# Performance work log

Measured on AMD Instinct MI355X. Metric: run time of the kernel, lower is better.

Reference implementation:

```python
import jax, jax.numpy as jnp
import numpy as np

NOTES = 8192
NPB = 8          # notes per beat (max buffer size for beat attention)
BPM = 4          # beats per measure
BEATS = NOTES // NPB
MEAS = BEATS // BPM
NOTE_D = 512     # note.size*2 (bidirectional encoder output)
BEAT_D = 512     # beat.size*2
MEAS_D = 256     # measure.size*2
ENC = 128        # encoder.size
TEMPO_H = 256    # beat.size
FINAL_H = 256    # final.size
OUT = 11         # output_size
RES_D = 8        # 5 + 3
NEG = -1e30


def lstm_cell(x, h, c, Wih, Whh, b):
    z = x @ Wih.T + h @ Whh.T + b
    i, f, g, o = jnp.split(z, 4)
    c = jax.nn.sigmoid(f) * c + jax.nn.sigmoid(i) * jnp.tanh(g)
    h = jax.nn.sigmoid(o) * jnp.tanh(c)
    return h, c


def setup_inputs():
    key = jax.random.key(0)
    ks = iter(jax.random.split(key, 40))
    def rn(shape, s=1.0):
        return jax.random.normal(next(ks), shape, jnp.float32) * s
    TEMPO_IN = BEAT_D + MEAS_D + 1 + RES_D + (OUT - 1) + ENC  # 915
    FINAL_IN = NOTE_D + BEAT_D + MEAS_D + OUT + ENC           # 1419
    return {
        'note_emb': rn((1, NOTES, NOTE_D)),
        'beat_emb': rn((1, BEATS, BEAT_D)),
        'measure_emb': rn((1, MEAS, MEAS_D)),
        'perf_embedding': rn((1, 64)),
        'res_info': rn((1, BEATS, RES_D)),
        'sve_W': rn((ENC, 64), 0.05), 'sve_b': rn((ENC,), 0.05),
        'psm_Wih': rn((4 * ENC, MEAS_D + ENC), 0.05),
        'psm_Whh': rn((4 * ENC, ENC), 0.05),
        'psm_b': rn((4 * ENC,), 0.05),
        'mpf_W': rn((ENC, ENC), 0.05), 'mpf_b': rn((ENC,), 0.05),
        'att_W': rn((OUT - 1, OUT - 1), 0.05), 'att_b': rn((OUT - 1,), 0.05),
        'att_c': rn((OUT - 1,), 0.5),
        'tempo_Wih': rn((4 * TEMPO_H, TEMPO_IN), 0.05),
        'tempo_Whh': rn((4 * TEMPO_H, TEMPO_H), 0.05),
        'tempo_b': rn((4 * TEMPO_H,), 0.05),
        'tempo_fc_W': rn((1, TEMPO_H), 0.05), 'tempo_fc_b': rn((1,), 0.05),
        'out_Wih': rn((4 * FINAL_H, FINAL_IN), 0.05),
        'out_Whh': rn((4 * FINAL_H, FINAL_H), 0.05),
        'out_b': rn((4 * FINAL_H,), 0.05),
        'fc_W': rn((OUT - 1, FINAL_H), 0.05), 'fc_b': rn((OUT - 1,), 0.05),
        'beat_numbers': jnp.arange(NOTES, dtype=jnp.int32) // NPB,
        'measure_numbers': jnp.arange(NOTES, dtype=jnp.int32) // (NPB * BPM),
        'edges': jnp.zeros((1,), jnp.int32),
    }


def _forward(note_emb, beat_emb, measure_emb, perf_embedding, res_info,
             sve_W, sve_b, psm_Wih, psm_Whh, psm_b, mpf_W, mpf_b,
             att_W, att_b, att_c, tempo_Wih, tempo_Whh, tempo_b,
             tempo_fc_W, tempo_fc_b, out_Wih, out_Whh, out_b, fc_W, fc_b,
             beat_numbers, measure_numbers):
    dt = note_emb.dtype
    b_idx = beat_numbers - beat_numbers[0]
    m_idx = measure_numbers - measure_numbers[0]
    nbuf = att_W.shape[0]  # output_size - 1

    # style_vector_expandor (Dropout is identity at inference)
    z = jax.nn.relu(perf_embedding.reshape(-1) @ sve_W.T + sve_b)  # [ENC]

    # perform_style_to_measure LSTM over measures, then measure_perf_fc
    meas = measure_emb[0]  # [M, MEAS_D]
    pzm = jnp.concatenate([jnp.broadcast_to(z, (meas.shape[0], z.shape[0])), meas], axis=1)
    h0 = jnp.zeros(psm_Whh.shape[1], dt)
    def mstep(carry, x):
        h, c = carry
        h, c = lstm_cell(x, h, c, psm_Wih, psm_Whh, psm_b)
        return (h, c), h
    _, mps = jax.lax.scan(mstep, (h0, h0), pzm)
    mps = mps @ mpf_W.T + mpf_b  # [M, ENC] measure_perform_style

    # gather per-note context (pure memory traffic)
    beat_pn = beat_emb[0][b_idx]
    meas_pn = meas[m_idx]
    mps_pn = mps[m_idx]
    res_pn = res_info[0][b_idx]
    notes = note_emb[0]
    is_start = jnp.concatenate([jnp.ones((1,), bool), b_idx[1:] > b_idx[:-1]])

    th0 = jnp.zeros(tempo_Whh.shape[1], dt)
    fh0 = jnp.zeros(out_Whh.shape[1], dt)
    carry0 = (th0, th0, fh0, fh0, jnp.zeros((1,), dt), jnp.zeros((OUT,), dt),
              jnp.zeros((NPB, nbuf), dt), jnp.zeros((), jnp.int32))

    def step(carry, xs):
        th, tc, fh, fcc, prev_tempo, prev_out, buf, cnt = carry
        n_e, b_e, m_e, mp, r_e, start = xs
        # --- beat boundary: ContextAttention (1 head) over previous beat's fc outputs
        mask = jnp.arange(NPB) < cnt
        scores = jnp.tanh(buf @ att_W.T + att_b) @ att_c  # [NPB]
        w = jax.nn.softmax(jnp.where(mask, scores, NEG))
        result = jnp.where(cnt > 0, w @ buf, jnp.zeros((nbuf,), dt))
        cat_t = jnp.concatenate([b_e, m_e, prev_tempo, r_e, result, mp])
        nth, ntc = lstm_cell(cat_t, th, tc, tempo_Wih, tempo_Whh, tempo_b)
        new_tempo = nth @ tempo_fc_W.T + tempo_fc_b  # [1]
        th = jnp.where(start, nth, th)
        tc = jnp.where(start, ntc, tc)
        prev_tempo = jnp.where(start, new_tempo, prev_tempo)
        buf = jnp.where(start, jnp.zeros_like(buf), buf)
        cnt = jnp.where(start, 0, cnt)
        # --- per-note output LSTM step
        cat_o = jnp.concatenate([n_e, b_e, m_e, prev_out, mp])
        fh, fcc = lstm_cell(cat_o, fh, fcc, out_Wih, out_Whh, out_b)
        o = fh @ fc_W.T + fc_b  # [OUT-1]
        buf = buf.at[cnt].set(o)
        out = jnp.concatenate([prev_tempo, o])  # QPM_INDEX = 0
        return (th, tc, fh, fcc, prev_tempo, out, buf, cnt + 1), out

    _, outs = jax.lax.scan(step, carry0, (notes, beat_pn, meas_pn, mps_pn, res_pn, is_start))
    return outs[None]  # [1, NOTES, OUT]


def reference(note_emb, beat_emb, measure_emb, perf_embedding, res_info,
              sve_W, sve_b, psm_Wih, psm_Whh, psm_b, mpf_W, mpf_b,
              att_W, att_b, att_c, tempo_Wih, tempo_Whh, tempo_b,
              tempo_fc_W, tempo_fc_b, out_Wih, out_Whh, out_b, fc_W, fc_b,
              beat_numbers, measure_numbers, edges):
    return _forward(note_emb, beat_emb, measure_emb, perf_embedding, res_info,
                    sve_W, sve_b, psm_Wih, psm_Whh, psm_b, mpf_W, mpf_b,
                    att_W, att_b, att_c, tempo_Wih, tempo_Whh, tempo_b,
                    tempo_fc_W, tempo_fc_b, out_Wih, out_Whh, out_b, fc_W, fc_b,
                    beat_numbers, measure_numbers)
```

## Files before the change

### kernel.cpp

```cpp
#include <hip/hip_runtime.h>
#include <cstdint>
#include <cstddef>

typedef _Float16 f16;
typedef _Float16 f16x2 __attribute__((ext_vector_type(2)));

__device__ __forceinline__ uint32_t packf16(float a, float b) {
  union { f16x2 h; uint32_t u; } u;
  u.h.x = (f16)a; u.h.y = (f16)b;
  return u.u;
}

__device__ __forceinline__ float fdot2(uint32_t a, uint32_t b, float c) {
#if __has_builtin(__builtin_amdgcn_fdot2)
  union { uint32_t u; f16x2 h; } ua, ub;
  ua.u = a; ub.u = b;
  return __builtin_amdgcn_fdot2(ua.h, ub.h, c, false);
#else
  union { uint32_t u; f16x2 h; } ua, ub;
  ua.u = a; ub.u = b;
  return c + (float)ua.h.x * (float)ub.h.x + (float)ua.h.y * (float)ub.h.y;
#endif
}

__device__ __forceinline__ float sigm_f(float x) { return 1.f / (1.f + __expf(-x)); }
__device__ __forceinline__ float tanh_f(float x) { float e = __expf(2.f * x); return 1.f - 2.f / (e + 1.f); }

__device__ __forceinline__ int acq_load(int* p) {
  return __hip_atomic_load(p, __ATOMIC_ACQUIRE, __HIP_MEMORY_SCOPE_AGENT);
}
__device__ __forceinline__ void rel_store(int* p, int v) {
  __hip_atomic_store(p, v, __ATOMIC_RELEASE, __HIP_MEMORY_SCOPE_AGENT);
}
__device__ __forceinline__ float rlx_loadf(float* p) {
  return __hip_atomic_load(p, __ATOMIC_RELAXED, __HIP_MEMORY_SCOPE_AGENT);
}
__device__ __forceinline__ void rlx_storef(float* p, float v) {
  __hip_atomic_store(p, v, __ATOMIC_RELAXED, __HIP_MEMORY_SCOPE_AGENT);
}

#define NOTES 8192
#define BEATS 1024
#define MEAS  256
#define KO    1440
#define KT    928

#define OFF_MB_NOTE   0
#define OFF_MB_TCNT   256
#define OFF_MB_O      512
#define OFF_MB_T      4096
#define OFF_ZSVE      8192
#define OFF_PM        16384
#define OFF_HM        540672
#define OFF_MPS       671744
#define OFF_XO        802816
#define OFF_WO        24395776
#define OFF_XT        27344896
#define OFF_WT        29245440
#define OFF_OPRE      31145984
#define OFF_TPRE      64700416

__global__ void k_sve(const float* __restrict__ perf, const float* __restrict__ W,
                      const float* __restrict__ b, float* __restrict__ z) {
  int j = threadIdx.x;
  float acc = b[j];
  for (int k = 0; k < 64; ++k) acc += perf[k] * W[j * 64 + k];
  z[j] = fmaxf(acc, 0.f);
}

__global__ __launch_bounds__(512) void k_pm(const float* __restrict__ z, const float* __restrict__ meas,
                                            const float* __restrict__ Wih, const float* __restrict__ b,
                                            float* __restrict__ Pm) {
  int m = blockIdx.x, r = threadIdx.x;
  __shared__ float x[384];
  for (int k = threadIdx.x; k < 384; k += 512)
    x[k] = (k < 128) ? z[k] : meas[m * 256 + (k - 128)];
  __syncthreads();
  const float* w = Wih + (size_t)r * 384;
  float acc = b[r];
  for (int k = 0; k < 384; ++k) acc += x[k] * w[k];
  Pm[(size_t)m * 512 + r] = acc;
}

__global__ __launch_bounds__(512) void k_psm_scan(const float* __restrict__ Pm,
                                                  const float* __restrict__ Whh,
                                                  float* __restrict__ hm) {
  int t = threadIdx.x;
  uint32_t w[64];
  {
    const float* wr = Whh + (size_t)t * 128;
#pragma unroll
    for (int k = 0; k < 64; ++k) w[k] = packf16(wr[2 * k], wr[2 * k + 1]);
  }
  __shared__ float z[512], c[128];
  __shared__ uint32_t h2[64];
  if (t < 128) c[t] = 0.f;
  if (t < 64) h2[t] = 0u;
  __syncthreads();
  for (int m = 0; m < 256; ++m) {
    float acc = Pm[(size_t)m * 512 + t];
    const uint4* h4 = (const uint4*)h2;
#pragma unroll
    for (int q = 0; q < 16; ++q) {
      uint4 hv = h4[q];
      acc = fdot2(w[4 * q + 0], hv.x, acc);
      acc = fdot2(w[4 * q + 1], hv.y, acc);
      acc = fdot2(w[4 * q + 2], hv.z, acc);
      acc = fdot2(w[4 * q + 3], hv.w, acc);
    }
    z[t] = acc;
    __syncthreads();
    if (t < 128) {
      float ig = sigm_f(z[t]), fg = sigm_f(z[128 + t]);
      float gg = tanh_f(z[256 + t]), og = sigm_f(z[384 + t]);
      float cn = fg * c[t] + ig * gg;
      c[t] = cn;
      float h = og * tanh_f(cn);
      hm[(size_t)m * 128 + t] = h;
      ((f16*)h2)[t] = (f16)h;
    }
    __syncthreads();
  }
}

__global__ void k_mps(const float* __restrict__ hm, const float* __restrict__ W,
                      const float* __restrict__ b, float* __restrict__ mps) {
  int m = blockIdx.x, j = threadIdx.x;
  const float* h = hm + (size_t)m * 128;
  const float* w = W + (size_t)j * 128;
  float acc = b[j];
  for (int k = 0; k < 128; ++k) acc += h[k] * w[k];
  mps[(size_t)m * 128 + j] = acc;
}

__global__ void k_build_xo(const float* __restrict__ notes, const float* __restrict__ beats,
                           const float* __restrict__ meas, const float* __restrict__ mps,
                           const int* __restrict__ bn, const int* __restrict__ mn,
                           f16* __restrict__ Xo) {
  int n = blockIdx.x;
  int b = bn[n] - bn[0], m = mn[n] - mn[0];
  f16* dst = Xo + (size_t)n * KO;
  for (int k = threadIdx.x; k < KO; k += 256) {
    float v;
    if (k < 512) v = notes[(size_t)n * 512 + k];
    else if (k < 1024) v = beats[(size_t)b * 512 + (k - 512)];
    else if (k < 1280) v = meas[(size_t)m * 256 + (k - 1024)];
    else if (k < 1291) v = 0.f;
    else if (k < 1419) v = mps[(size_t)m * 128 + (k - 1291)];
    else v = 0.f;
    dst[k] = (f16)v;
  }
}

__global__ void k_build_xt(const float* __restrict__ beats, const float* __restrict__ meas,
                           const float* __restrict__ res, const float* __restrict__ mps,
                           const int* __restrict__ bn, const int* __restrict__ mn,
                           f16* __restrict__ Xt) {
  int b = blockIdx.x;
  int n0 = b * 8;
  int be = bn[n0] - bn[0], m = mn[n0] - mn[0];
  f16* dst = Xt + (size_t)b * KT;
  for (int k = threadIdx.x; k < KT; k += 256) {
    float v;
    if (k < 512) v = beats[(size_t)be * 512 + k];
    else if (k < 768) v = meas[(size_t)m * 256 + (k - 512)];
    else if (k == 768) v = 0.f;
    else if (k < 777) v = res[(size_t)be * 8 + (k - 769)];
    else if (k < 787) v = 0.f;
    else if (k < 915) v = mps[(size_t)m * 128 + (k - 787)];
    else v = 0.f;
    dst[k] = (f16)v;
  }
}

__global__ void k_build_w(const float* __restrict__ W, f16* __restrict__ Wf, int K, int Kpad) {
  int r = blockIdx.x;
  for (int k = threadIdx.x; k < Kpad; k += 256)
    Wf[(size_t)r * Kpad + k] = (f16)((k < K) ? W[(size_t)r * K + k] : 0.f);
}

#define LDS_STRIDE 36
__global__ __launch_bounds__(256) void k_gemm(const f16* __restrict__ X, const f16* __restrict__ W,
                                              const float* __restrict__ bias, float* __restrict__ C,
                                              int ktiles, int ldx, int ldw) {
  __shared__ f16 Xs[64 * LDS_STRIDE];
  __shared__ f16 Ws[64 * LDS_STRIDE];
  int t = threadIdx.x;
  int tx = t & 15, ty = t >> 4;
  int row0 = blockIdx.y * 64, col0 = blockIdx.x * 64;
  int lr = t >> 2;
  int lc = (t & 3) * 8;
  const f16* xsrc = X + (size_t)(row0 + lr) * ldx + lc;
  const f16* wsrc = W + (size_t)(col0 + lr) * ldw + lc;
  float acc[4][4] = {{0.f}};
  for (int kb = 0; kb < ktiles; ++kb) {
    uint4 xa = *(const uint4*)(xsrc + (size_t)kb * 32);
    uint4 wa = *(const uint4*)(wsrc + (size_t)kb * 32);
    __syncthreads();
    *(uint2*)(Xs + lr * LDS_STRIDE + lc) = make_uint2(xa.x, xa.y);
    *(uint2*)(Xs + lr * LDS_STRIDE + lc + 4) = make_uint2(xa.z, xa.w);
    *(uint2*)(Ws + lr * LDS_STRIDE + lc) = make_uint2(wa.x, wa.y);
    *(uint2*)(Ws + lr * LDS_STRIDE + lc + 4) = make_uint2(wa.z, wa.w);
    __syncthreads();
#pragma unroll
    for (int kk = 0; kk < 8; ++kk) {
      uint2 av[4], bv[4];
#pragma unroll
      for (int i = 0; i < 4; ++i) av[i] = *(const uint2*)(Xs + (ty * 4 + i) * LDS_STRIDE + kk * 4);
#pragma unroll
      for (int j = 0; j < 4; ++j) bv[j] = *(const uint2*)(Ws + (tx * 4 + j) * LDS_STRIDE + kk * 4);
#pragma unroll
      for (int i = 0; i < 4; ++i)
#pragma unroll
        for (int j = 0; j < 4; ++j) {
          acc[i][j] = fdot2(av[i].x, bv[j].x, acc[i][j]);
          acc[i][j] = fdot2(av[i].y, bv[j].y, acc[i][j]);
        }
    }
  }
#pragma unroll
  for (int i = 0; i < 4; ++i)
#pragma unroll
    for (int j = 0; j < 4; ++j) {
      int cc = col0 + tx * 4 + j;
      C[(size_t)(row0 + ty * 4 + i) * 1024 + cc] = acc[i][j] + bias[cc];
    }
}

#define WL_BYTES 131072
#define REGQ 24
#define LDSQ 8

#define FCW_STRIDE 264

struct S0 {
  float z[1024];
  float h_f32[256];
  uint32_t h2[128];
  float c[256];
  float o_prev[12];
  float fcW[10 * FCW_STRIDE];
  float fcb[16];
};
struct S1 {
  float z[1024];
  float th_f32[256];
  uint32_t th2[128];
  float tc[256];
  float tfcW[256];
  float tfcb[4];
  float attW[100];
  float attb[12];
  float attc[12];
  float buf[8][10];
  float scp[8][10];
  float sc[8];
  float wsm[8];
  float result[12];
  float prev_t[4];
};
union SU { S0 s0; S1 s1; };
#define DYN_LDS (WL_BYTES + sizeof(SU) + 256)

__device__ __forceinline__ void dot_pair(const uint32_t* w0, const uint32_t* w1,
                                         const uint2* __restrict__ wl, int t,
                                         const uint32_t* __restrict__ h2,
                                         float& a0, float& a1) {
  const uint4* h4 = (const uint4*)h2;
#pragma unroll
  for (int q = 0; q < REGQ; ++q) {
    uint4 hv = h4[q];
    a0 = fdot2(w0[4 * q + 0], hv.x, a0); a1 = fdot2(w1[4 * q + 0], hv.x, a1);
    a0 = fdot2(w0[4 * q + 1], hv.y, a0); a1 = fdot2(w1[4 * q + 1], hv.y, a1);
    a0 = fdot2(w0[4 * q + 2], hv.z, a0); a1 = fdot2(w1[4 * q + 2], hv.z, a1);
    a0 = fdot2(w0[4 * q + 3], hv.w, a0); a1 = fdot2(w1[4 * q + 3], hv.w, a1);
  }
#pragma unroll
  for (int q = 0; q < LDSQ; ++q) {
    uint4 hv = h4[REGQ + q];
    uint2 p0 = wl[(4 * q + 0) * 512 + t];
    uint2 p1 = wl[(4 * q + 1) * 512 + t];
    uint2 p2 = wl[(4 * q + 2) * 512 + t];
    uint2 p3 = wl[(4 * q + 3) * 512 + t];
    a0 = fdot2(p0.x, hv.x, a0); a1 = fdot2(p0.y, hv.x, a1);
    a0 = fdot2(p1.x, hv.y, a0); a1 = fdot2(p1.y, hv.y, a1);
    a0 = fdot2(p2.x, hv.z, a0); a1 = fdot2(p2.y, hv.z, a1);
    a0 = fdot2(p3.x, hv.w, a0); a1 = fdot2(p3.y, hv.w, a1);
  }
}

__global__
__attribute__((amdgpu_flat_work_group_size(512, 512)))
__attribute__((amdgpu_waves_per_eu(2, 2)))
void k_scan(
    const float* __restrict__ O_pre, const float* __restrict__ T_pre,
    const float* __restrict__ out_Whh, const float* __restrict__ out_Wih,
    const float* __restrict__ fc_W, const float* __restrict__ fc_b,
    const float* __restrict__ tempo_Whh, const float* __restrict__ tempo_Wih,
    const float* __restrict__ tempo_fc_W, const float* __restrict__ tempo_fc_b,
    const float* __restrict__ att_W, const float* __restrict__ att_b,
    const float* __restrict__ att_c,
    float* __restrict__ dout,
    int* mb_note_cnt, int* mb_tempo_cnt, float* mb_o, float* mb_tempo) {
  extern __shared__ __align__(16) char dsm[];
  uint2* wl2 = (uint2*)dsm;
  SU* S = (SU*)(dsm + WL_BYTES);
  int t = threadIdx.x;

  if (blockIdx.x == 0) {
    uint32_t w0[4 * REGQ], w1[4 * REGQ];
    float wpo0[11], wpo1[11];
    {
      const float* r0p = out_Whh + (size_t)t * 256;
      const float* r1p = out_Whh + (size_t)(t + 512) * 256;
#pragma unroll
      for (int k = 0; k < 4 * REGQ; ++k) {
        w0[k] = packf16(r0p[2 * k], r0p[2 * k + 1]);
        w1[k] = packf16(r1p[2 * k], r1p[2 * k + 1]);
      }
      for (int k = 0; k < 32; ++k)
        wl2[k * 512 + t] = make_uint2(packf16(r0p[192 + 2 * k], r0p[193 + 2 * k]),
                                      packf16(r1p[192 + 2 * k], r1p[193 + 2 * k]));
      for (int j = 0; j < 11; ++j) {
        wpo0[j] = out_Wih[(size_t)t * 1419 + 1280 + j];
        wpo1[j] = out_Wih[(size_t)(t + 512) * 1419 + 1280 + j];
      }
    }
    for (int i = t; i < 10 * FCW_STRIDE; i += 512) {
      int j = i / FCW_STRIDE, k = i - j * FCW_STRIDE;
      S->s0.fcW[i] = (k < 256) ? fc_W[j * 256 + k] : 0.f;
    }
    if (t < 16) S->s0.fcb[t] = (t < 10) ? fc_b[t] : 0.f;
    if (t < 128) S->s0.h2[t] = 0u;
    if (t < 256) S->s0.c[t] = 0.f;
    if (t < 12) S->s0.o_prev[t] = 0.f;
    __syncthreads();

    float p0 = O_pre[t];
    float p1 = O_pre[t + 512];
    for (int n = 0; n < NOTES; ++n) {
      int nn = (n + 1 < NOTES) ? n + 1 : n;
      float pn0 = O_pre[(size_t)nn * 1024 + t];
      float pn1 = O_pre[(size_t)nn * 1024 + t + 512];
      float a0 = p0, a1 = p1;
      dot_pair(w0, w1, wl2, t, S->s0.h2, a0, a1);
#pragma unroll
      for (int j = 0; j < 11; ++j) {
        float ov = S->s0.o_prev[j];
        a0 += wpo0[j] * ov;
        a1 += wpo1[j] * ov;
      }
      S->s0.z[t] = a0;
      S->s0.z[t + 512] = a1;
      __syncthreads();
      if (t < 256) {
        float ig = sigm_f(S->s0.z[t]);
        float fg = sigm_f(S->s0.z[256 + t]);
        float gg = tanh_f(S->s0.z[512 + t]);
        float og = sigm_f(S->s0.z[768 + t]);
        float cn = fg * S->s0.c[t] + ig * gg;
        S->s0.c[t] = cn;
        float h = og * tanh_f(cn);
        S->s0.h_f32[t] = h;
        ((f16*)S->s0.h2)[t] = (f16)h;
      }
      __syncthreads();
      if (t < 160) {
        int j = t >> 4, l = t & 15;
        const float* fw = &S->s0.fcW[j * FCW_STRIDE + l];
        const float* hp = &S->s0.h_f32[l];
        float s = 0.f;
#pragma unroll
        for (int i = 0; i < 16; ++i) s += fw[i * 16] * hp[i * 16];
        s += __shfl_xor(s, 1, 16);
        s += __shfl_xor(s, 2, 16);
        s += __shfl_xor(s, 4, 16);
        s += __shfl_xor(s, 8, 16);
        if (l == 0) {
          float oj = s + S->s0.fcb[j];
          dout[(size_t)n * 11 + 1 + j] = oj;
          rlx_storef(&mb_o[(n & 15) * 10 + j], oj);
          S->s0.o_prev[1 + j] = oj;
        }
      }
      __syncthreads();
      int r = n & 7;
      if ((r == 0) | (r == 7)) {
        if (t == 0) {
          if (r == 7) rel_store(mb_note_cnt, n + 1);
          else {
            int b = n >> 3;
            while (acq_load(mb_tempo_cnt) < b + 1) __builtin_amdgcn_s_sleep(2);
            S->s0.o_prev[0] = rlx_loadf(&mb_tempo[b]);
          }
        }
        if (r == 0) __syncthreads();
      }
      p0 = pn0;
      p1 = pn1;
    }
  } else {
    uint32_t w0[4 * REGQ], w1[4 * REGQ];
    float wres0[10], wres1[10], wpt0, wpt1;
    {
      const float* r0p = tempo_Whh + (size_t)t * 256;
      const float* r1p = tempo_Whh + (size_t)(t + 512) * 256;
#pragma unroll
      for (int k = 0; k < 4 * REGQ; ++k) {
        w0[k] = packf16(r0p[2 * k], r0p[2 * k + 1]);
        w1[k] = packf16(r1p[2 * k], r1p[2 * k + 1]);
      }
      for (int k = 0; k < 32; ++k)
        wl2[k * 512 + t] = make_uint2(packf16(r0p[192 + 2 * k], r0p[193 + 2 * k]),
                                      packf16(r1p[192 + 2 * k], r1p[193 + 2 * k]));
      wpt0 = tempo_Wih[(size_t)t * 915 + 768];
      wpt1 = tempo_Wih[(size_t)(t + 512) * 915 + 768];
      for (int j = 0; j < 10; ++j) {
        wres0[j] = tempo_Wih[(size_t)t * 915 + 777 + j];
        wres1[j] = tempo_Wih[(size_t)(t + 512) * 915 + 777 + j];
      }
    }
    if (t < 256) S->s1.tfcW[t] = tempo_fc_W[t];
    if (t < 4) S->s1.tfcb[t] = tempo_fc_b[0];
    if (t < 100) S->s1.attW[t] = att_W[t];
    if (t < 10) { S->s1.attb[t] = att_b[t]; S->s1.attc[t] = att_c[t]; }
    if (t < 128) S->s1.th2[t] = 0u;
    if (t < 256) S->s1.tc[t] = 0.f;
    if (t < 12) S->s1.result[t] = 0.f;
    if (t < 4) S->s1.prev_t[t] = 0.f;
    __syncthreads();

    for (int b = 0; b < BEATS; ++b) {
      float q0 = T_pre[(size_t)b * 1024 + t];
      float q1 = T_pre[(size_t)b * 1024 + t + 512];
      if (b > 0) {
        if (t == 0) {
          while (acq_load(mb_note_cnt) < 8 * b) __builtin_amdgcn_s_sleep(2);
        }
        __syncthreads();
        if (t < 80) {
          int i = t / 10, j = t % 10;
          S->s1.buf[i][j] = rlx_loadf(&mb_o[(((b - 1) * 8 + i) & 15) * 10 + j]);
        }
        __syncthreads();
        if (t < 80) {
          int i = t / 10, j = t % 10;
          float s = S->s1.attb[j];
          for (int k = 0; k < 10; ++k) s += S->s1.buf[i][k] * S->s1.attW[j * 10 + k];
          S->s1.scp[i][j] = tanh_f(s) * S->s1.attc[j];
        }
        __syncthreads();
        if (t < 8) {
          float s = 0.f;
          for (int j = 0; j < 10; ++j) s += S->s1.scp[t][j];
          S->s1.sc[t] = s;
        }
        __syncthreads();
        if (t == 0) {
          float m = -1e30f;
          for (int i = 0; i < 8; ++i) m = fmaxf(m, S->s1.sc[i]);
          float e[8], ssum = 0.f;
          for (int i = 0; i < 8; ++i) { e[i] = __expf(S->s1.sc[i] - m); ssum += e[i]; }
          for (int i = 0; i < 8; ++i) S->s1.wsm[i] = e[i] / ssum;
        }
        __syncthreads();
        if (t < 10) {
          float r = 0.f;
          for (int i = 0; i < 8; ++i) r += S->s1.wsm[i] * S->s1.buf[i][t];
          S->s1.result[t] = r;
        }
        __syncthreads();
      }
      float a0 = q0, a1 = q1;
      dot_pair(w0, w1, wl2, t, S->s1.th2, a0, a1);
      float pt = S->s1.prev_t[0];
      a0 += wpt0 * pt;
      a1 += wpt1 * pt;
#pragma unroll
      for (int j = 0; j < 10; ++j) {
        float rv = S->s1.result[j];
        a0 += wres0[j] * rv;
        a1 += wres1[j] * rv;
      }
      S->s1.z[t] = a0;
      S->s1.z[t + 512] = a1;
      __syncthreads();
      if (t < 256) {
        float ig = sigm_f(S->s1.z[t]);
        float fg = sigm_f(S->s1.z[256 + t]);
        float gg = tanh_f(S->s1.z[512 + t]);
        float og = sigm_f(S->s1.z[768 + t]);
        float cn = fg * S->s1.tc[t] + ig * gg;
        S->s1.tc[t] = cn;
        float h = og * tanh_f(cn);
        S->s1.th_f32[t] = h;
        ((f16*)S->s1.th2)[t] = (f16)h;
      }
      __syncthreads();
      if (t < 64) {
        float4 hv = *(const float4*)&S->s1.th_f32[t * 4];
        float4 wv = *(const float4*)&S->s1.tfcW[t * 4];
        float v = wv.x * hv.x + wv.y * hv.y + wv.z * hv.z + wv.w * hv.w;
        v += __shfl_xor(v, 1);
        v += __shfl_xor(v, 2);
        v += __shfl_xor(v, 4);
        v += __shfl_xor(v, 8);
        v += __shfl_xor(v, 16);
        v += __shfl_xor(v, 32);
        float nt = v + S->s1.tfcb[0];
        if (t == 0) {
          rlx_storef(&mb_tempo[b], nt);
          S->s1.prev_t[0] = nt;
          rel_store(mb_tempo_cnt, b + 1);
        }
        if (t < 8) dout[(size_t)(8 * b + t) * 11] = nt;
      }
      __syncthreads();
    }
  }
}

extern "C" void kernel_launch(void* const* d_in, const int* in_sizes, int n_in,
                              void* d_out, int out_size, void* d_ws, size_t ws_size,
                              hipStream_t stream) {
  const float* note_emb   = (const float*)d_in[0];
  const float* beat_emb   = (const float*)d_in[1];
  const float* measure_emb= (const float*)d_in[2];
  const float* perf_emb   = (const float*)d_in[3];
  const float* res_info   = (const float*)d_in[4];
  const float* sve_W      = (const float*)d_in[5];
  const float* sve_b      = (const float*)d_in[6];
  const float* psm_Wih    = (const float*)d_in[7];
  const float* psm_Whh    = (const float*)d_in[8];
  const float* psm_b      = (const float*)d_in[9];
  const float* mpf_W      = (const float*)d_in[10];
  const float* mpf_b      = (const float*)d_in[11];
  const float* att_W      = (const float*)d_in[12];
  const float* att_b      = (const float*)d_in[13];
  const float* att_c      = (const float*)d_in[14];
  const float* tempo_Wih  = (const float*)d_in[15];
  const float* tempo_Whh  = (const float*)d_in[16];
  const float* tempo_b    = (const float*)d_in[17];
  const float* tempo_fc_W = (const float*)d_in[18];
  const float* tempo_fc_b = (const float*)d_in[19];
  const float* out_Wih    = (const float*)d_in[20];
  const float* out_Whh    = (const float*)d_in[21];
  const float* out_b      = (const float*)d_in[22];
  const float* fc_W       = (const float*)d_in[23];
  const float* fc_b       = (const float*)d_in[24];
  const int*   bn         = (const int*)d_in[25];
  const int*   mn         = (const int*)d_in[26];
  float* out = (float*)d_out;

  char* ws = (char*)d_ws;
  int*   mb_note = (int*)(ws + OFF_MB_NOTE);
  int*   mb_tcnt = (int*)(ws + OFF_MB_TCNT);
  float* mb_o    = (float*)(ws + OFF_MB_O);
  float* mb_t    = (float*)(ws + OFF_MB_T);
  float* z_sve   = (float*)(ws + OFF_ZSVE);
  float* Pm      = (float*)(ws + OFF_PM);
  float* hm      = (float*)(ws + OFF_HM);
  float* mps     = (float*)(ws + OFF_MPS);
  f16*   Xo      = (f16*)(ws + OFF_XO);
  f16*   Wo      = (f16*)(ws + OFF_WO);
  f16*   Xt      = (f16*)(ws + OFF_XT);
  f16*   Wt      = (f16*)(ws + OFF_WT);
  float* O_pre   = (float*)(ws + OFF_OPRE);
  float* T_pre   = (float*)(ws + OFF_TPRE);

  k_sve<<<1, 128, 0, stream>>>(perf_emb, sve_W, sve_b, z_sve);
  k_pm<<<256, 512, 0, stream>>>(z_sve, measure_emb, psm_Wih, psm_b, Pm);
  k_psm_scan<<<1, 512, 0, stream>>>(Pm, psm_Whh, hm);
  k_mps<<<256, 128, 0, stream>>>(hm, mpf_W, mpf_b, mps);
  k_build_xo<<<NOTES, 256, 0, stream>>>(note_emb, beat_emb, measure_emb, mps, bn, mn, Xo);
  k_build_w<<<1024, 256, 0, stream>>>(out_Wih, Wo, 1419, KO);
  k_build_xt<<<BEATS, 256, 0, stream>>>(beat_emb, measure_emb, res_info, mps, bn, mn, Xt);
  k_build_w<<<1024, 256, 0, stream>>>(tempo_Wih, Wt, 915, KT);
  k_gemm<<<dim3(16, 128), 256, 0, stream>>>(Xo, Wo, out_b, O_pre, KO / 32, KO, KO);
  k_gemm<<<dim3(16, 16), 256, 0, stream>>>(Xt, Wt, tempo_b, T_pre, KT / 32, KT, KT);

  hipFuncSetAttribute(reinterpret_cast<const void*>(k_scan),
                      hipFuncAttributeMaxDynamicSharedMemorySize, (int)DYN_LDS);
  k_scan<<<2, 512, DYN_LDS, stream>>>(O_pre, T_pre, out_Whh, out_Wih, fc_W, fc_b,
                                      tempo_Whh, tempo_Wih, tempo_fc_W, tempo_fc_b,
                                      att_W, att_c ? att_b : att_b, att_c, out,
                                      mb_note, mb_tcnt, mb_o, mb_t);
}
```

Before: 28.28 ms.

## Use 1024 threads per recurrent block with readlane broadcast of hidden state

The sequential LSTM scan blocks now run 1024 threads, one gate row per thread instead of two. Each thread loads a slice of the f16 hidden state once and broadcasts it with readlane, rather than having every thread read the full vector from LDS. The cell state moves into registers, and the small extra inputs (previous outputs, tempo, attention result) are packed as f16 pairs and applied with fdot2. This roughly halves the per-thread serial dot-product length and cuts LDS traffic per step. In exchange there are more waves to synchronise at each barrier, register pressure is high, and the extra inputs lose precision by going to f16.

```diff
diff --git a/kernel.cpp b/kernel.cpp
--- a/kernel.cpp
+++ b/kernel.cpp
@@ -21,6 +21,10 @@
   ua.u = a; ub.u = b;
   return c + (float)ua.h.x * (float)ub.h.x + (float)ua.h.y * (float)ub.h.y;
 #endif
+}
+
+__device__ __forceinline__ uint32_t rl(uint32_t v, int lane) {
+  return (uint32_t)__builtin_amdgcn_readlane((int)v, lane);
 }
 
 __device__ __forceinline__ float sigm_f(float x) { return 1.f / (1.f + __expf(-x)); }
@@ -228,8 +232,6 @@
 }
 
 #define WL_BYTES 131072
-#define REGQ 24
-#define LDSQ 8
 
 #define FCW_STRIDE 264
 
@@ -237,8 +239,7 @@
   float z[1024];
   float h_f32[256];
   uint32_t h2[128];
-  float c[256];
-  float o_prev[12];
+  uint32_t o2[8];
   float fcW[10 * FCW_STRIDE];
   float fcb[16];
 };
@@ -246,7 +247,7 @@
   float z[1024];
   float th_f32[256];
   uint32_t th2[128];
-  float tc[256];
+  uint32_t res2[8];
   float tfcW[256];
   float tfcb[4];
   float attW[100];
@@ -256,42 +257,36 @@
   float scp[8][10];
   float sc[8];
   float wsm[8];
-  float result[12];
-  float prev_t[4];
 };
 union SU { S0 s0; S1 s1; };
 #define DYN_LDS (WL_BYTES + sizeof(SU) + 256)
 
-__device__ __forceinline__ void dot_pair(const uint32_t* w0, const uint32_t* w1,
-                                         const uint2* __restrict__ wl, int t,
-                                         const uint32_t* __restrict__ h2,
-                                         float& a0, float& a1) {
-  const uint4* h4 = (const uint4*)h2;
-#pragma unroll
-  for (int q = 0; q < REGQ; ++q) {
-    uint4 hv = h4[q];
-    a0 = fdot2(w0[4 * q + 0], hv.x, a0); a1 = fdot2(w1[4 * q + 0], hv.x, a1);
-    a0 = fdot2(w0[4 * q + 1], hv.y, a0); a1 = fdot2(w1[4 * q + 1], hv.y, a1);
-    a0 = fdot2(w0[4 * q + 2], hv.z, a0); a1 = fdot2(w1[4 * q + 2], hv.z, a1);
-    a0 = fdot2(w0[4 * q + 3], hv.w, a0); a1 = fdot2(w1[4 * q + 3], hv.w, a1);
-  }
-#pragma unroll
-  for (int q = 0; q < LDSQ; ++q) {
-    uint4 hv = h4[REGQ + q];
-    uint2 p0 = wl[(4 * q + 0) * 512 + t];
-    uint2 p1 = wl[(4 * q + 1) * 512 + t];
-    uint2 p2 = wl[(4 * q + 2) * 512 + t];
-    uint2 p3 = wl[(4 * q + 3) * 512 + t];
-    a0 = fdot2(p0.x, hv.x, a0); a1 = fdot2(p0.y, hv.x, a1);
-    a0 = fdot2(p1.x, hv.y, a0); a1 = fdot2(p1.y, hv.y, a1);
-    a0 = fdot2(p2.x, hv.z, a0); a1 = fdot2(p2.y, hv.z, a1);
-    a0 = fdot2(p3.x, hv.w, a0); a1 = fdot2(p3.y, hv.w, a1);
-  }
+__device__ __forceinline__ float dot_row(const uint32_t* w, const uint4* __restrict__ wl,
+                                         int t, uint4 hs, float a0) {
+#pragma unroll
+  for (int q = 0; q < 24; ++q) {
+    uint32_t s0 = rl(hs.x, q), s1 = rl(hs.y, q), s2 = rl(hs.z, q), s3 = rl(hs.w, q);
+    a0 = fdot2(w[4 * q + 0], s0, a0);
+    a0 = fdot2(w[4 * q + 1], s1, a0);
+    a0 = fdot2(w[4 * q + 2], s2, a0);
+    a0 = fdot2(w[4 * q + 3], s3, a0);
+  }
+#pragma unroll
+  for (int q = 0; q < 8; ++q) {
+    uint4 wv = wl[q * 1024 + t];
+    int c = 24 + q;
+    uint32_t s0 = rl(hs.x, c), s1 = rl(hs.y, c), s2 = rl(hs.z, c), s3 = rl(hs.w, c);
+    a0 = fdot2(wv.x, s0, a0);
+    a0 = fdot2(wv.y, s1, a0);
+    a0 = fdot2(wv.z, s2, a0);
+    a0 = fdot2(wv.w, s3, a0);
+  }
+  return a0;
 }
 
 __global__
-__attribute__((amdgpu_flat_work_group_size(512, 512)))
-__attribute__((amdgpu_waves_per_eu(2, 2)))
+__attribute__((amdgpu_flat_work_group_size(1024, 1024)))
+__attribute__((amdgpu_waves_per_eu(4)))
 void k_scan(
     const float* __restrict__ O_pre, const float* __restrict__ T_pre,
     const float* __restrict__ out_Whh, const float* __restrict__ out_Wih,
@@ -303,64 +298,54 @@
     float* __restrict__ dout,
     int* mb_note_cnt, int* mb_tempo_cnt, float* mb_o, float* mb_tempo) {
   extern __shared__ __align__(16) char dsm[];
-  uint2* wl2 = (uint2*)dsm;
+  uint4* wl4 = (uint4*)dsm;
   SU* S = (SU*)(dsm + WL_BYTES);
   int t = threadIdx.x;
 
   if (blockIdx.x == 0) {
-    uint32_t w0[4 * REGQ], w1[4 * REGQ];
-    float wpo0[11], wpo1[11];
+    uint32_t w[96], wpo2[6];
     {
-      const float* r0p = out_Whh + (size_t)t * 256;
-      const float* r1p = out_Whh + (size_t)(t + 512) * 256;
-#pragma unroll
-      for (int k = 0; k < 4 * REGQ; ++k) {
-        w0[k] = packf16(r0p[2 * k], r0p[2 * k + 1]);
-        w1[k] = packf16(r1p[2 * k], r1p[2 * k + 1]);
-      }
-      for (int k = 0; k < 32; ++k)
-        wl2[k * 512 + t] = make_uint2(packf16(r0p[192 + 2 * k], r0p[193 + 2 * k]),
-                                      packf16(r1p[192 + 2 * k], r1p[193 + 2 * k]));
-      for (int j = 0; j < 11; ++j) {
-        wpo0[j] = out_Wih[(size_t)t * 1419 + 1280 + j];
-        wpo1[j] = out_Wih[(size_t)(t + 512) * 1419 + 1280 + j];
-      }
-    }
-    for (int i = t; i < 10 * FCW_STRIDE; i += 512) {
+      const float* wr = out_Whh + (size_t)t * 256;
+#pragma unroll
+      for (int k = 0; k < 96; ++k) w[k] = packf16(wr[2 * k], wr[2 * k + 1]);
+#pragma unroll
+      for (int q = 0; q < 8; ++q)
+        wl4[q * 1024 + t] = make_uint4(packf16(wr[192 + 8 * q], wr[193 + 8 * q]),
+                                       packf16(wr[194 + 8 * q], wr[195 + 8 * q]),
+                                       packf16(wr[196 + 8 * q], wr[197 + 8 * q]),
+                                       packf16(wr[198 + 8 * q], wr[199 + 8 * q]));
+      const float* wih = out_Wih + (size_t)t * 1419 + 1280;
+#pragma unroll
+      for (int j = 0; j < 5; ++j) wpo2[j] = packf16(wih[2 * j], wih[2 * j + 1]);
+      wpo2[5] = packf16(wih[10], 0.f);
+    }
+    for (int i = t; i < 10 * FCW_STRIDE; i += 1024) {
       int j = i / FCW_STRIDE, k = i - j * FCW_STRIDE;
       S->s0.fcW[i] = (k < 256) ? fc_W[j * 256 + k] : 0.f;
     }
     if (t < 16) S->s0.fcb[t] = (t < 10) ? fc_b[t] : 0.f;
     if (t < 128) S->s0.h2[t] = 0u;
-    if (t < 256) S->s0.c[t] = 0.f;
-    if (t < 12) S->s0.o_prev[t] = 0.f;
+    if (t < 8) S->s0.o2[t] = 0u;
+    float creg = 0.f;
     __syncthreads();
 
-    float p0 = O_pre[t];
-    float p1 = O_pre[t + 512];
+    float p = O_pre[t];
     for (int n = 0; n < NOTES; ++n) {
       int nn = (n + 1 < NOTES) ? n + 1 : n;
-      float pn0 = O_pre[(size_t)nn * 1024 + t];
-      float pn1 = O_pre[(size_t)nn * 1024 + t + 512];
-      float a0 = p0, a1 = p1;
-      dot_pair(w0, w1, wl2, t, S->s0.h2, a0, a1);
-#pragma unroll
-      for (int j = 0; j < 11; ++j) {
-        float ov = S->s0.o_prev[j];
-        a0 += wpo0[j] * ov;
-        a1 += wpo1[j] * ov;
-      }
+      float pn = O_pre[(size_t)nn * 1024 + t];
+      uint4 hs = *(const uint4*)(S->s0.h2 + 4 * (t & 31));
+      float a0 = dot_row(w, wl4, t, hs, p);
+#pragma unroll
+      for (int j = 0; j < 6; ++j) a0 = fdot2(wpo2[j], S->s0.o2[j], a0);
       S->s0.z[t] = a0;
-      S->s0.z[t + 512] = a1;
       __syncthreads();
       if (t < 256) {
         float ig = sigm_f(S->s0.z[t]);
         float fg = sigm_f(S->s0.z[256 + t]);
         float gg = tanh_f(S->s0.z[512 + t]);
         float og = sigm_f(S->s0.z[768 + t]);
-        float cn = fg * S->s0.c[t] + ig * gg;
-        S->s0.c[t] = cn;
-        float h = og * tanh_f(cn);
+        creg = fg * creg + ig * gg;
+        float h = og * tanh_f(creg);
         S->s0.h_f32[t] = h;
         ((f16*)S->s0.h2)[t] = (f16)h;
       }
@@ -380,7 +365,7 @@
           float oj = s + S->s0.fcb[j];
           dout[(size_t)n * 11 + 1 + j] = oj;
           rlx_storef(&mb_o[(n & 15) * 10 + j], oj);
-          S->s0.o_prev[1 + j] = oj;
+          ((f16*)S->s0.o2)[1 + j] = (f16)oj;
         }
       }
       __syncthreads();
@@ -391,48 +376,41 @@
           else {
             int b = n >> 3;
             while (acq_load(mb_tempo_cnt) < b + 1) __builtin_amdgcn_s_sleep(2);
-            S->s0.o_prev[0] = rlx_loadf(&mb_tempo[b]);
+            ((f16*)S->s0.o2)[0] = (f16)rlx_loadf(&mb_tempo[b]);
           }
         }
         if (r == 0) __syncthreads();
       }
-      p0 = pn0;
-      p1 = pn1;
+      p = pn;
     }
   } else {
-    uint32_t w0[4 * REGQ], w1[4 * REGQ];
-    float wres0[10], wres1[10], wpt0, wpt1;
+    uint32_t w[96], wdt2[6];
     {
-      const float* r0p = tempo_Whh + (size_t)t * 256;
-      const float* r1p = tempo_Whh + (size_t)(t + 512) * 256;
-#pragma unroll
-      for (int k = 0; k < 4 * REGQ; ++k) {
-        w0[k] = packf16(r0p[2 * k], r0p[2 * k + 1]);
-        w1[k] = packf16(r1p[2 * k], r1p[2 * k + 1]);
-      }
-      for (int k = 0; k < 32; ++k)
-        wl2[k * 512 + t] = make_uint2(packf16(r0p[192 + 2 * k], r0p[193 + 2 * k]),
-                                      packf16(r1p[192 + 2 * k], r1p[193 + 2 * k]));
-      wpt0 = tempo_Wih[(size_t)t * 915 + 768];
-      wpt1 = tempo_Wih[(size_t)(t + 512) * 915 + 768];
-      for (int j = 0; j < 10; ++j) {
-        wres0[j] = tempo_Wih[(size_t)t * 915 + 777 + j];
-        wres1[j] = tempo_Wih[(size_t)(t + 512) * 915 + 777 + j];
-      }
+      const float* wr = tempo_Whh + (size_t)t * 256;
+#pragma unroll
+      for (int k = 0; k < 96; ++k) w[k] = packf16(wr[2 * k], wr[2 * k + 1]);
+#pragma unroll
+      for (int q = 0; q < 8; ++q)
+        wl4[q * 1024 + t] = make_uint4(packf16(wr[192 + 8 * q], wr[193 + 8 * q]),
+                                       packf16(wr[194 + 8 * q], wr[195 + 8 * q]),
+                                       packf16(wr[196 + 8 * q], wr[197 + 8 * q]),
+                                       packf16(wr[198 + 8 * q], wr[199 + 8 * q]));
+      const float* twih = tempo_Wih + (size_t)t * 915;
+      wdt2[0] = packf16(twih[768], twih[777]);
+#pragma unroll
+      for (int j = 1; j < 5; ++j) wdt2[j] = packf16(twih[776 + 2 * j], twih[777 + 2 * j]);
+      wdt2[5] = packf16(twih[786], 0.f);
     }
     if (t < 256) S->s1.tfcW[t] = tempo_fc_W[t];
     if (t < 4) S->s1.tfcb[t] = tempo_fc_b[0];
     if (t < 100) S->s1.attW[t] = att_W[t];
     if (t < 10) { S->s1.attb[t] = att_b[t]; S->s1.attc[t] = att_c[t]; }
     if (t < 128) S->s1.th2[t] = 0u;
-    if (t < 256) S->s1.tc[t] = 0.f;
-    if (t < 12) S->s1.result[t] = 0.f;
-    if (t < 4) S->s1.prev_t[t] = 0.f;
+    if (t < 8) S->s1.res2[t] = 0u;
+    float creg = 0.f;
     __syncthreads();
 
     for (int b = 0; b < BEATS; ++b) {
-      float q0 = T_pre[(size_t)b * 1024 + t];
-      float q1 = T_pre[(size_t)b * 1024 + t + 512];
       if (b > 0) {
         if (t == 0) {
           while (acq_load(mb_note_cnt) < 8 * b) __builtin_amdgcn_s_sleep(2);
@@ -467,32 +445,24 @@
         if (t < 10) {
           float r = 0.f;
           for (int i = 0; i < 8; ++i) r += S->s1.wsm[i] * S->s1.buf[i][t];
-          S->s1.result[t] = r;
+          ((f16*)S->s1.res2)[1 + t] = (f16)r;
         }
         __syncthreads();
       }
-      float a0 = q0, a1 = q1;
-      dot_pair(w0, w1, wl2, t, S->s1.th2, a0, a1);
-      float pt = S->s1.prev_t[0];
-      a0 += wpt0 * pt;
-      a1 += wpt1 * pt;
-#pragma unroll
-      for (int j = 0; j < 10; ++j) {
-        float rv = S->s1.result[j];
-        a0 += wres0[j] * rv;
-        a1 += wres1[j] * rv;
-      }
+      float q0 = T_pre[(size_t)b * 1024 + t];
+      uint4 hs = *(const uint4*)(S->s1.th2 + 4 * (t & 31));
+      float a0 = dot_row(w, wl4, t, hs, q0);
+#pragma unroll
+      for (int j = 0; j < 6; ++j) a0 = fdot2(wdt2[j], S->s1.res2[j], a0);
       S->s1.z[t] = a0;
-      S->s1.z[t + 512] = a1;
       __syncthreads();
       if (t < 256) {
         float ig = sigm_f(S->s1.z[t]);
         float fg = sigm_f(S->s1.z[256 + t]);
         float gg = tanh_f(S->s1.z[512 + t]);
         float og = sigm_f(S->s1.z[768 + t]);
-        float cn = fg * S->s1.tc[t] + ig * gg;
-        S->s1.tc[t] = cn;
-        float h = og * tanh_f(cn);
+        creg = fg * creg + ig * gg;
+        float h = og * tanh_f(creg);
         S->s1.th_f32[t] = h;
         ((f16*)S->s1.th2)[t] = (f16)h;
       }
@@ -510,7 +480,7 @@
         float nt = v + S->s1.tfcb[0];
         if (t == 0) {
           rlx_storef(&mb_tempo[b], nt);
-          S->s1.prev_t[0] = nt;
+          ((f16*)S->s1.res2)[0] = (f16)nt;
           rel_store(mb_tempo_cnt, b + 1);
         }
         if (t < 8) dout[(size_t)(8 * b + t) * 11] = nt;
@@ -581,8 +551,8 @@
 
   hipFuncSetAttribute(reinterpret_cast<const void*>(k_scan),
                       hipFuncAttributeMaxDynamicSharedMemorySize, (int)DYN_LDS);
-  k_scan<<<2, 512, DYN_LDS, stream>>>(O_pre, T_pre, out_Whh, out_Wih, fc_W, fc_b,
-                                      tempo_Whh, tempo_Wih, tempo_fc_W, tempo_fc_b,
-                                      att_W, att_c ? att_b : att_b, att_c, out,
-                                      mb_note, mb_tcnt, mb_o, mb_t);
-}
+  k_scan<<<2, 1024, DYN_LDS, stream>>>(O_pre, T_pre, out_Whh, out_Wih, fc_W, fc_b,
+                                       tempo_Whh, tempo_Wih, tempo_fc_W, tempo_fc_b,
+                                       att_W, att_b, att_c, out,
+                                       mb_note, mb_tcnt, mb_o, mb_t);
+}
```

Result: slower. 29.46 ms (+4.1%).
